# Kernel optimization log

Hardware: AMD Instinct MI355X
Metric: run time of the kernel (lower is better)

The kernel has to match this reference:

```python
import jax, jax.numpy as jnp
import numpy as np

N = 30000   # nodes
E = 300000  # edges
B = 64      # graphs
H = 4       # heads
C = 64      # channels per head
HC = H * C  # 256


def setup_inputs() -> dict:
    key = jax.random.key(0)
    ks = jax.random.split(key, 32)

    def rn(k, shape):
        scale = 1.0 / np.sqrt(shape[0])
        return (jax.random.normal(k, shape) * scale).astype(jnp.float32)

    inp = {}
    inp["x"] = jax.random.normal(ks[0], (N, 13), dtype=jnp.float32)
    inp["edge_index"] = jax.random.randint(ks[1], (2, E), 0, N, dtype=jnp.int64)
    inp["edge_attr"] = jax.random.normal(ks[2], (E, 51), dtype=jnp.float32)
    inp["batch"] = jnp.sort(jax.random.randint(ks[3], (N,), 0, B, dtype=jnp.int64))
    # init node MLP: Linear(13 -> 128) (plain_last => no act/norm)
    inp["W0"] = rn(ks[4], (13, 128)); inp["b0"] = jnp.zeros((128,), jnp.float32)
    # GATv2 layer 1: in 128 -> H=4, C=64
    inp["Wl1"] = rn(ks[5], (128, HC)); inp["bl1"] = jnp.zeros((HC,), jnp.float32)
    inp["Wr1"] = rn(ks[6], (128, HC)); inp["br1"] = jnp.zeros((HC,), jnp.float32)
    inp["We1"] = rn(ks[7], (51, HC))
    inp["att1"] = rn(ks[8], (H, C))
    inp["bias1"] = jnp.zeros((HC,), jnp.float32)
    # GATv2 layer 2: in 256 -> H=4, C=64
    inp["Wl2"] = rn(ks[9], (HC, HC)); inp["bl2"] = jnp.zeros((HC,), jnp.float32)
    inp["Wr2"] = rn(ks[10], (HC, HC)); inp["br2"] = jnp.zeros((HC,), jnp.float32)
    inp["We2"] = rn(ks[11], (51, HC))
    inp["att2"] = rn(ks[12], (H, C))
    inp["bias2"] = jnp.zeros((HC,), jnp.float32)
    # attention pooling MLP: Linear(256 -> 256) (plain_last)
    inp["Wp"] = rn(ks[13], (HC, HC)); inp["bp"] = jnp.zeros((HC,), jnp.float32)
    # out MLP: Linear(256->256)+BN+ReLU, Linear(256->2001)
    inp["Wo1"] = rn(ks[14], (HC, 256)); inp["bo1"] = jnp.zeros((256,), jnp.float32)
    inp["gamma"] = jnp.ones((256,), jnp.float32); inp["beta"] = jnp.zeros((256,), jnp.float32)
    inp["Wo2"] = rn(ks[15], (256, 2001)); inp["bo2"] = jnp.zeros((2001,), jnp.float32)
    return inp


def _gatv2(x, src, dst, ea, Wl, bl, Wr, br, We, att, bias):
    n = x.shape[0]
    xl = (x @ Wl + bl).reshape(n, H, C)   # source transform (also message content)
    xr = (x @ Wr + br).reshape(n, H, C)   # target transform
    ee = (ea @ We).reshape(-1, H, C)      # edge embedding, no bias
    z = jax.nn.leaky_relu(xl[src] + xr[dst] + ee, negative_slope=0.2)  # [E,H,C]
    logit = jnp.einsum('ehc,hc->eh', z, att)                           # [E,H]
    m = jax.ops.segment_max(logit, dst, num_segments=n)                # [N,H]
    w = jnp.exp(logit - m[dst])
    den = jax.ops.segment_sum(w, dst, num_segments=n)
    alpha = w / (den[dst] + 1e-16)                                     # segment softmax
    out = jax.ops.segment_sum(xl[src] * alpha[:, :, None], dst, num_segments=n)
    return out.reshape(n, HC) + bias


def _forward(x, edge_index, edge_attr, batch, W0, b0, Wl1, bl1, Wr1, br1, We1, att1, bias1,
             Wl2, bl2, Wr2, br2, We2, att2, bias2, Wp, bp, Wo1, bo1, gamma, beta, Wo2, bo2):
    src, dst = edge_index[0], edge_index[1]
    h = x @ W0 + b0
    h = _gatv2(h, src, dst, edge_attr, Wl1, bl1, Wr1, br1, We1, att1, bias1)
    h = _gatv2(h, src, dst, edge_attr, Wl2, bl2, Wr2, br2, We2, att2, bias2)
    # softmax attention pooling over nodes of each graph (per feature column)
    a = h @ Wp + bp                                       # [N,HC]
    am = jax.ops.segment_max(a, batch, num_segments=B)
    aw = jnp.exp(a - am[batch])
    ad = jax.ops.segment_sum(aw, batch, num_segments=B)
    attw = aw / (ad[batch] + 1e-16)
    g = jax.ops.segment_sum(h * attw, batch, num_segments=B)  # [B,HC]
    # out MLP: Linear + BatchNorm(train stats) + ReLU + Linear, then leaky_relu
    y = g @ Wo1 + bo1
    mu = jnp.mean(y, axis=0)
    var = jnp.var(y, axis=0)
    y = (y - mu) / jnp.sqrt(var + 1e-5) * gamma + beta
    y = jax.nn.relu(y)
    y = y @ Wo2 + bo2
    return jax.nn.leaky_relu(y, negative_slope=0.01)


def reference(x, edge_index, edge_attr, batch, W0, b0, Wl1, bl1, Wr1, br1, We1, att1, bias1,
              Wl2, bl2, Wr2, br2, We2, att2, bias2, Wp, bp, Wo1, bo1, gamma, beta, Wo2, bo2):
    return _forward(x, edge_index, edge_attr, batch, W0, b0, Wl1, bl1, Wr1, br1, We1, att1, bias1,
                    Wl2, bl2, Wr2, br2, We2, att2, bias2, Wp, bp, Wo1, bo1, gamma, beta, Wo2, bo2)
```

## Files before the change

### kernel.cpp

```cpp
#include <hip/hip_runtime.h>
#include <hip/hip_bf16.h>

#define NN 30000
#define EE 300000
#define BB 64
#define HH 4
#define CC 64
#define HC 256

typedef __attribute__((ext_vector_type(8))) short short8;
typedef __attribute__((ext_vector_type(4))) float floatx4;

__device__ __forceinline__ float b2f(short x) {
    return __uint_as_float(((unsigned)(unsigned short)x) << 16);
}
__device__ __forceinline__ unsigned short f2b(float f) {
    __hip_bfloat16 h = __float2bfloat16(f);
    return *(unsigned short*)&h;
}

#define GLD16(gp, lp) __builtin_amdgcn_global_load_lds( \
    (const __attribute__((address_space(1))) void*)(gp), \
    (__attribute__((address_space(3))) void*)(lp), 16, 0, 0)

#define ROT2(x) ((((x) << 2) | ((x) >> 3)) & 31)
#define EESWZ(chunk, row) (ROT2(chunk) ^ (((row) >> 2) & 3) ^ (((row) & 1) << 2))

template<int CT>
__global__ __launch_bounds__(256) void mfma_gemm(
    const ushort* __restrict__ A, const ushort* __restrict__ Bt,
    const float* __restrict__ bias, float* __restrict__ outF,
    __hip_bfloat16* __restrict__ outB, int M, int Nc, int K) {
    constexpr int SMEM_USHORTS =
        ((64 * 32 + CT * 64 * 32) > (64 * CT * 64)) ? (64 * 32 + CT * 64 * 32)
                                                    : (64 * CT * 64);
    __shared__ __align__(16) ushort smem[SMEM_USHORTS];
    ushort* lA = smem;
    ushort* lB = smem + 64 * 32;
    const int tid = threadIdx.x, lane = tid & 63, wv = tid >> 6;
    const int row0 = blockIdx.x * 64, col0 = blockIdx.y * (CT * 64);

    floatx4 acc[4][CT];
#pragma unroll
    for (int r = 0; r < 4; r++)
#pragma unroll
        for (int c = 0; c < CT; c++) acc[r][c] = (floatx4){0.f, 0.f, 0.f, 0.f};

    const int arow = tid >> 2;
    const int sl   = (tid & 3) ^ ((tid >> 3) & 3);
    const ushort* ga = A + (size_t)(row0 + arow) * K + sl * 8;
    const int m16 = lane & 15, q = lane >> 4;

    for (int k0 = 0; k0 < K; k0 += 32) {
        __syncthreads();
        GLD16(ga + k0, &lA[tid * 8]);
#pragma unroll
        for (int j = 0; j < CT; j++) {
            const ushort* gb = Bt + (size_t)(col0 + j * 64 + arow) * K + k0 + sl * 8;
            GLD16(gb, &lB[j * 2048 + tid * 8]);
        }
        __syncthreads();
        short8 aF[4], bF[CT];
#pragma unroll
        for (int r = 0; r < 4; r++) {
            int rr = r * 16 + m16;
            aF[r] = *(const short8*)&lA[rr * 32 + ((q ^ ((rr >> 1) & 3)) << 3)];
        }
#pragma unroll
        for (int c = 0; c < CT; c++) {
            int nr = (wv * CT + c) * 16 + m16;
            bF[c] = *(const short8*)&lB[nr * 32 + ((q ^ ((nr >> 1) & 3)) << 3)];
        }
#pragma unroll
        for (int r = 0; r < 4; r++)
#pragma unroll
            for (int c = 0; c < CT; c++)
                acc[r][c] = __builtin_amdgcn_mfma_f32_16x16x32_bf16(aF[r], bF[c], acc[r][c], 0, 0, 0);
    }

    if (outB != nullptr) {
        __syncthreads();
#pragma unroll
        for (int c = 0; c < CT; c++) {
            int lcol = (wv * CT + c) * 16 + m16;
            float bv = bias ? bias[col0 + lcol] : 0.f;
            int ch = lcol >> 3, c7 = lcol & 7;
#pragma unroll
            for (int r = 0; r < 4; r++)
#pragma unroll
                for (int j = 0; j < 4; j++) {
                    int row = r * 16 + q * 4 + j;
                    smem[row * (CT * 64) + ((ch ^ (row & 7)) << 3) + c7] =
                        f2b(acc[r][c][j] + bv);
                }
        }
        __syncthreads();
        constexpr int SH = (CT == 4) ? 5 : 4;
#pragma unroll
        for (int s = 0; s < CT * 2; s++) {
            int g = tid + 256 * s;
            int row = g >> SH, ch = g & (CT * 8 - 1);
            int grow = row0 + row;
            if (grow < M) {
                short8 v = *(const short8*)&smem[row * (CT * 64) + ((ch ^ (row & 7)) << 3)];
                *(short8*)((ushort*)outB + (size_t)grow * Nc + col0 + ch * 8) = v;
            }
        }
    } else {
#pragma unroll
        for (int c = 0; c < CT; c++) {
            int col = col0 + (wv * CT + c) * 16 + m16;
            float bv = bias ? bias[col] : 0.f;
#pragma unroll
            for (int r = 0; r < 4; r++)
#pragma unroll
                for (int j = 0; j < 4; j++) {
                    int row = row0 + r * 16 + q * 4 + j;
                    if (row < M) outF[(size_t)row * Nc + col] = acc[r][c][j] + bv;
                }
        }
    }
}

__global__ void permute_ea_frag(const float* __restrict__ ea,
                                const int* __restrict__ eidx,
                                ushort* __restrict__ ea_frag) {
    const int t = threadIdx.x, tile = blockIdx.x;
    const int r  = t >> 6;
    const int ch = (t >> 3) & 7;
    if (ch == 7) return;
    const int m0 = (t * 2) & 15;
    ushort* outp = ea_frag + (size_t)tile * 4096 + t * 16;
#pragma unroll
    for (int half = 0; half < 2; half++) {
        int row = r * 16 + m0 + half;
        int gi = tile * 64 + row;
        int e = (gi < EE) ? eidx[gi] : -1;
        short8 v8;
#pragma unroll
        for (int j = 0; j < 8; j++) {
            int k = ch * 8 + j;
            float v = (e >= 0 && k < 51) ? ea[(size_t)e * 51 + k] : 0.f;
            v8[j] = (short)f2b(v);
        }
        *(short8*)(outp + half * 8) = v8;
    }
}

__global__ void pack_we_frag(const float* __restrict__ WeA,
                             const float* __restrict__ WeB,
                             ushort* __restrict__ WfA, ushort* __restrict__ WfB) {
    const float* We = blockIdx.y ? WeB : WeA;
    ushort* Wf = blockIdx.y ? WfB : WfA;
    int o = blockIdx.x * 256 + threadIdx.x;
    int j = o & 7, m16 = (o >> 3) & 15, ch = (o >> 7) & 7, nt = o >> 10;
    int n = nt * 16 + m16, k = ch * 8 + j;
    float v = (k < 51) ? We[k * 256 + n] : 0.f;
    Wf[o] = f2b(v);
}

__global__ __launch_bounds__(256, 4) void edge_fused(
    const ushort* __restrict__ ea_frag, const ushort* __restrict__ Wfrag,
    const float* __restrict__ att,
    const int* __restrict__ src_csr, const int* __restrict__ dst_csr,
    const ushort* __restrict__ xlr, float* __restrict__ logitp) {
    __shared__ __align__(16) ushort eeS[64 * 256];
    __shared__ float satt[256];
    const int tid = threadIdx.x, lane = tid & 63, wv = tid >> 6;
    const int tile = ((int)blockIdx.x & 7) * 586 + ((int)blockIdx.x >> 3);
    const int i0 = tile * 64;
    satt[tid] = att[tid];
    const int m16 = lane & 15, q = lane >> 4;

    floatx4 acc[4][4];
#pragma unroll
    for (int r = 0; r < 4; r++)
#pragma unroll
        for (int c = 0; c < 4; c++) acc[r][c] = (floatx4){0.f, 0.f, 0.f, 0.f};

    short8 zz;
#pragma unroll
    for (int z = 0; z < 8; z++) zz[z] = 0;

    const ushort* af = ea_frag + (size_t)tile * 4096;
#pragma unroll
    for (int k0 = 0; k0 < 2; k0++) {
        short8 aF[4], bF[4];
        const bool live = !(k0 == 1 && q == 3);
        if (live) {
#pragma unroll
            for (int r = 0; r < 4; r++)
                aF[r] = *(const short8*)&af[((r * 8 + k0 * 4 + q) * 16 + m16) * 8];
#pragma unroll
            for (int c = 0; c < 4; c++)
                bF[c] = *(const short8*)&Wfrag[(((wv * 4 + c) * 8 + k0 * 4 + q) * 16 + m16) * 8];
        } else {
#pragma unroll
            for (int r = 0; r < 4; r++) aF[r] = zz;
#pragma unroll
            for (int c = 0; c < 4; c++) bF[c] = zz;
        }
#pragma unroll
        for (int r = 0; r < 4; r++)
#pragma unroll
            for (int c = 0; c < 4; c++)
                acc[r][c] = __builtin_amdgcn_mfma_f32_16x16x32_bf16(aF[r], bF[c], acc[r][c], 0, 0, 0);
    }

#pragma unroll
    for (int r = 0; r < 4; r++)
#pragma unroll
        for (int cc = 0; cc < 4; cc++)
#pragma unroll
            for (int j = 0; j < 4; j++) {
                int row = r * 16 + q * 4 + j;
                int col = (wv * 4 + cc) * 16 + m16;
                int chunk = col >> 3;
                int P = EESWZ(chunk, row);
                eeS[row * 256 + (P << 3) + (col & 7)] = f2b(acc[r][cc][j]);
            }
    __syncthreads();

    const int el = tid >> 2, h = tid & 3;
    const int i = i0 + el;
    if (i < EE) {
        int src = src_csr[i], dstn = dst_csr[i];
        const ushort* xlp = xlr + (size_t)src * 512 + h * 64;
        const ushort* xrp = xlr + (size_t)dstn * 512 + 256 + h * 64;
        float s = 0.f;
#pragma unroll
        for (int c = 0; c < 8; c++) {
            short8 xlv = *(const short8*)(xlp + c * 8);
            short8 xrv = *(const short8*)(xrp + c * 8);
            int chunk = h * 8 + c;
            int P = EESWZ(chunk, el);
            short8 eev = *(const short8*)&eeS[el * 256 + (P << 3)];
#pragma unroll
            for (int j = 0; j < 8; j++) {
                float v = b2f(xlv[j]) + b2f(xrv[j]) + b2f(eev[j]);
                v = v > 0.f ? v : 0.2f * v;
                s += v * satt[h * 64 + c * 8 + j];
            }
        }
        logitp[(size_t)i * 4 + h] = s;
    }
}

__global__ void pack_x(const float* __restrict__ x, __hip_bfloat16* __restrict__ d,
                       int* __restrict__ deg) {
    int i = blockIdx.x * 256 + threadIdx.x;
    if (i < NN) deg[i] = 0;
    if (i >= NN * 32) return;
    int n = i >> 5, k = i & 31;
    d[i] = __float2bfloat16(k < 13 ? x[n * 13 + k] : 0.f);
}
struct PackJob { const float* W; __hip_bfloat16* dst; int K, Nc, Kpad, rowoff; };
struct PackJobs { PackJob j[6]; };
__global__ void pack_all(PackJobs jobs) {
    PackJob jb = jobs.j[blockIdx.y];
    int tot = jb.Nc * jb.Kpad;
    for (int i = blockIdx.x * 256 + threadIdx.x; i < tot; i += gridDim.x * 256) {
        int n = i / jb.Kpad, k = i - n * jb.Kpad;
        float v = (k < jb.K) ? jb.W[k * jb.Nc + n] : 0.f;
        jb.dst[(size_t)(jb.rowoff + n) * jb.Kpad + k] = __float2bfloat16(v);
    }
}
__global__ void cat2(const float* __restrict__ a, const float* __restrict__ b,
                     float* __restrict__ o) {
    int i = blockIdx.x * 256 + threadIdx.x;
    if (i < 512) o[i] = i < 256 ? a[i] : b[i - 256];
}

__global__ void hist_deg(const int* __restrict__ ei, int* __restrict__ deg) {
    int e = blockIdx.x * 256 + threadIdx.x;
    if (e < EE) atomicAdd(&deg[ei[EE + e]], 1);
}
__global__ void scan1(const int* __restrict__ deg, int* __restrict__ partial,
                      int* __restrict__ bsum) {
    __shared__ int sh[256];
    int t = threadIdx.x, i = blockIdx.x * 256 + t;
    int v = (i < NN) ? deg[i] : 0;
    sh[t] = v; __syncthreads();
    for (int off = 1; off < 256; off <<= 1) {
        int x = (t >= off) ? sh[t - off] : 0;
        __syncthreads();
        sh[t] += x;
        __syncthreads();
    }
    if (i < NN) partial[i] = sh[t] - v;
    if (t == 255) bsum[blockIdx.x] = sh[255];
}
__global__ void scan2(int* __restrict__ bsum, int nb) {
    __shared__ int sh[256];
    int t = threadIdx.x;
    int v = (t < nb) ? bsum[t] : 0;
    sh[t] = v; __syncthreads();
    for (int off = 1; off < 256; off <<= 1) {
        int x = (t >= off) ? sh[t - off] : 0;
        __syncthreads();
        sh[t] += x;
        __syncthreads();
    }
    if (t < nb) bsum[t] = sh[t] - v;
}
__global__ void scan3(const int* __restrict__ partial, const int* __restrict__ bsum,
                      int* __restrict__ start, int* __restrict__ cursor) {
    int i = blockIdx.x * 256 + threadIdx.x;
    if (i < NN) { start[i] = partial[i] + bsum[i >> 8]; cursor[i] = 0; }
    else if (i == NN) start[NN] = EE;
}
__global__ void scatter_e(const int* __restrict__ ei, int* __restrict__ cursor,
                          const int* __restrict__ start, int* __restrict__ eidx,
                          int* __restrict__ src_csr, int* __restrict__ dst_csr) {
    int e = blockIdx.x * 256 + threadIdx.x;
    if (e >= EE) return;
    int s = ei[e];
    int d = ei[EE + e];
    int p = atomicAdd(&cursor[d], 1);
    int pos = start[d] + p;
    eidx[pos] = e;
    src_csr[pos] = s;
    dst_csr[pos] = d;
}

__global__ __launch_bounds__(256) void aggregate_csr(
    const ushort* __restrict__ xlr, const float* __restrict__ logitp,
    const int* __restrict__ src_csr, const int* __restrict__ start,
    const float* __restrict__ bias, ushort* __restrict__ outb) {
    const int lane = threadIdx.x & 63, wv = threadIdx.x >> 6;
    const int dst = blockIdx.x * 4 + wv;
    if (dst >= NN) return;
    const int s0 = start[dst];
    const int deg = start[dst + 1] - s0;
    const int h = lane >> 4;

    float m[4] = {-3.4e38f, -3.4e38f, -3.4e38f, -3.4e38f};
    float lg[4] = {0.f, 0.f, 0.f, 0.f};
    int mysrc = 0;
    if (lane < deg) {
        mysrc = src_csr[s0 + lane];
        float4 l4 = ((const float4*)logitp)[s0 + lane];
        lg[0] = l4.x; lg[1] = l4.y; lg[2] = l4.z; lg[3] = l4.w;
        m[0] = l4.x; m[1] = l4.y; m[2] = l4.z; m[3] = l4.w;
    }
    for (int i = 64 + lane; i < deg; i += 64) {
        float4 l4 = ((const float4*)logitp)[s0 + i];
        m[0] = fmaxf(m[0], l4.x); m[1] = fmaxf(m[1], l4.y);
        m[2] = fmaxf(m[2], l4.z); m[3] = fmaxf(m[3], l4.w);
    }
#pragma unroll
    for (int off = 32; off; off >>= 1)
#pragma unroll
        for (int k = 0; k < 4; k++) m[k] = fmaxf(m[k], __shfl_xor(m[k], off));

    float w[4], d[4];
#pragma unroll
    for (int k = 0; k < 4; k++) {
        w[k] = (lane < deg) ? __expf(lg[k] - m[k]) : 0.f;
        d[k] = w[k];
    }
    for (int i = 64 + lane; i < deg; i += 64) {
        float4 l4 = ((const float4*)logitp)[s0 + i];
        d[0] += __expf(l4.x - m[0]); d[1] += __expf(l4.y - m[1]);
        d[2] += __expf(l4.z - m[2]); d[3] += __expf(l4.w - m[3]);
    }
#pragma unroll
    for (int off = 32; off; off >>= 1)
#pragma unroll
        for (int k = 0; k < 4; k++) d[k] += __shfl_xor(d[k], off);
    const float dh = 1.f / (((h == 0) ? d[0] : (h == 1) ? d[1] : (h == 2) ? d[2] : d[3]) + 1e-16f);
    const float mh = (h == 0) ? m[0] : (h == 1) ? m[1] : (h == 2) ? m[2] : m[3];

    float4 b4 = ((const float4*)bias)[lane];
    float a0 = b4.x, a1 = b4.y, a2 = b4.z, a3 = b4.w;

    const int dcap = deg < 64 ? deg : 64;
    const ushort* xbase = xlr + (size_t)lane * 4;
    int i = 0;
    for (; i + 4 <= dcap; i += 4) {
        int sv[4]; float aw[4];
#pragma unroll
        for (int u = 0; u < 4; u++) {
            sv[u] = __shfl(mysrc, i + u);
            float s0v = __shfl(w[0], i + u), s1v = __shfl(w[1], i + u);
            float s2v = __shfl(w[2], i + u), s3v = __shfl(w[3], i + u);
            aw[u] = ((h == 0) ? s0v : (h == 1) ? s1v : (h == 2) ? s2v : s3v) * dh;
        }
        ushort4 xv[4];
#pragma unroll
        for (int u = 0; u < 4; u++)
            xv[u] = *(const ushort4*)(xbase + (size_t)sv[u] * 512);
#pragma unroll
        for (int u = 0; u < 4; u++) {
            a0 += b2f(xv[u].x) * aw[u]; a1 += b2f(xv[u].y) * aw[u];
            a2 += b2f(xv[u].z) * aw[u]; a3 += b2f(xv[u].w) * aw[u];
        }
    }
    for (; i < dcap; i++) {
        int srcv = __shfl(mysrc, i);
        float s0v = __shfl(w[0], i), s1v = __shfl(w[1], i);
        float s2v = __shfl(w[2], i), s3v = __shfl(w[3], i);
        float aw = ((h == 0) ? s0v : (h == 1) ? s1v : (h == 2) ? s2v : s3v) * dh;
        ushort4 xv = *(const ushort4*)(xbase + (size_t)srcv * 512);
        a0 += b2f(xv.x) * aw; a1 += b2f(xv.y) * aw;
        a2 += b2f(xv.z) * aw; a3 += b2f(xv.w) * aw;
    }
    for (int ii = 64; ii < deg; ii++) {
        int srcv = src_csr[s0 + ii];
        float4 l4 = ((const float4*)logitp)[s0 + ii];
        float lh = (h == 0) ? l4.x : (h == 1) ? l4.y : (h == 2) ? l4.z : l4.w;
        float aw = __expf(lh - mh) * dh;
        ushort4 xv = *(const ushort4*)(xbase + (size_t)srcv * 512);
        a0 += b2f(xv.x) * aw; a1 += b2f(xv.y) * aw;
        a2 += b2f(xv.z) * aw; a3 += b2f(xv.w) * aw;
    }
    ushort4 ov;
    ov.x = f2b(a0); ov.y = f2b(a1); ov.z = f2b(a2); ov.w = f2b(a3);
    *(ushort4*)(outb + (size_t)dst * 256 + lane * 4) = ov;
}

__device__ __forceinline__ unsigned fmap(float f) {
    unsigned u = __float_as_uint(f);
    return (u & 0x80000000u) ? ~u : (u | 0x80000000u);
}
__device__ __forceinline__ float funmap(unsigned u) {
    return (u & 0x80000000u) ? __uint_as_float(u & 0x7FFFFFFFu)
                             : __uint_as_float(~u);
}

__global__ void pool_max(const float* __restrict__ a, const int* __restrict__ batch,
                         unsigned* __restrict__ am, float* __restrict__ den,
                         float* __restrict__ num) {
    const int c = threadIdx.x;
    if (blockIdx.x < BB) {
        den[blockIdx.x * HC + c] = 0.f;
        num[blockIdx.x * HC + c] = 0.f;
    }
    const int n0 = blockIdx.x * 64;
    int curb = batch[n0];
    float m = -3.4e38f;
    const int nend = min(n0 + 64, NN);
    for (int n = n0; n < nend; n++) {
        int b = batch[n];
        float v = a[(size_t)n * HC + c];
        if (b != curb) { atomicMax(&am[curb * HC + c], fmap(m)); curb = b; m = v; }
        else           { m = fmaxf(m, v); }
    }
    atomicMax(&am[curb * HC + c], fmap(m));
}
__global__ void pool_sums(const float* __restrict__ a, const __hip_bfloat16* __restrict__ h2,
                          const int* __restrict__ batch, const unsigned* __restrict__ am,
                          float* __restrict__ den, float* __restrict__ num) {
    const int c = threadIdx.x;
    const int n0 = blockIdx.x * 64;
    int curb = batch[n0];
    float sd = 0.f, sn = 0.f;
    float mcur = funmap(am[curb * HC + c]);
    const int nend = min(n0 + 64, NN);
    for (int n = n0; n < nend; n++) {
        int b = batch[n];
        if (b != curb) {
            atomicAdd(&den[curb * HC + c], sd);
            atomicAdd(&num[curb * HC + c], sn);
            curb = b; sd = 0.f; sn = 0.f; mcur = funmap(am[b * HC + c]);
        }
        float w = __expf(a[(size_t)n * HC + c] - mcur);
        sd += w;
        sn += __bfloat162float(h2[(size_t)n * HC + c]) * w;
    }
    atomicAdd(&den[curb * HC + c], sd);
    atomicAdd(&num[curb * HC + c], sn);
}

__global__ void mlp_lin1(const float* __restrict__ num, const float* __restrict__ den,
                         const float* __restrict__ Wo1, const float* __restrict__ bo1,
                         float* __restrict__ y) {
    __shared__ float gsh[HC];
    const int c = threadIdx.x;
    const int r = blockIdx.x;
    gsh[c] = num[r * HC + c] / (den[r * HC + c] + 1e-16f);
    __syncthreads();
    float acc = bo1[c];
#pragma unroll 4
    for (int k = 0; k < HC; k++) acc = fmaf(gsh[k], Wo1[k * HC + c], acc);
    y[r * HC + c] = acc;
}
__global__ void bn_relu(float* __restrict__ y, const float* __restrict__ gamma,
                        const float* __restrict__ beta) {
    const int c = threadIdx.x;
    float s = 0.f, sq = 0.f;
    for (int r = 0; r < BB; r++) { float v = y[r * HC + c]; s += v; sq += v * v; }
    float mu  = s * (1.f / BB);
    float var = sq * (1.f / BB) - mu * mu;
    float inv = rsqrtf(var + 1e-5f) * gamma[c];
    float bt  = beta[c];
    for (int r = 0; r < BB; r++) {
        float v = (y[r * HC + c] - mu) * inv + bt;
        y[r * HC + c] = v > 0.f ? v : 0.f;
    }
}
__global__ void mlp_lin2(const float* __restrict__ y, const float* __restrict__ Wo2,
                         const float* __restrict__ bo2, float* __restrict__ out) {
    const int j = blockIdx.x * 256 + threadIdx.x;
    const int r = blockIdx.y;
    if (j >= 2001) return;
    float acc = bo2[j];
#pragma unroll 4
    for (int k = 0; k < HC; k++) acc = fmaf(y[r * HC + k], Wo2[k * 2001 + j], acc);
    out[r * 2001 + j] = acc > 0.f ? acc : 0.01f * acc;
}

extern "C" void kernel_launch(void* const* d_in, const int* in_sizes, int n_in,
                              void* d_out, int out_size, void* d_ws, size_t ws_size,
                              hipStream_t stream) {
    const float* x     = (const float*)d_in[0];
    const int*   ei    = (const int*)d_in[1];
    const float* ea    = (const float*)d_in[2];
    const int*   batch = (const int*)d_in[3];
    const float* W0 = (const float*)d_in[4];  const float* b0 = (const float*)d_in[5];
    const float* Wl1 = (const float*)d_in[6]; const float* bl1 = (const float*)d_in[7];
    const float* Wr1 = (const float*)d_in[8]; const float* br1 = (const float*)d_in[9];
    const float* We1 = (const float*)d_in[10]; const float* att1 = (const float*)d_in[11];
    const float* bias1 = (const float*)d_in[12];
    const float* Wl2 = (const float*)d_in[13]; const float* bl2 = (const float*)d_in[14];
    const float* Wr2 = (const float*)d_in[15]; const float* br2 = (const float*)d_in[16];
    const float* We2 = (const float*)d_in[17]; const float* att2 = (const float*)d_in[18];
    const float* bias2 = (const float*)d_in[19];
    const float* Wp = (const float*)d_in[20]; const float* bp = (const float*)d_in[21];
    const float* Wo1 = (const float*)d_in[22]; const float* bo1 = (const float*)d_in[23];
    const float* gamma = (const float*)d_in[24]; const float* beta = (const float*)d_in[25];
    const float* Wo2 = (const float*)d_in[26]; const float* bo2 = (const float*)d_in[27];
    float* out = (float*)d_out;

    char* p = (char*)d_ws;
    auto alloc = [&](size_t bytes) { char* r = p; p += (bytes + 255) & ~(size_t)255; return r; };
    const int MP = 30016;
    const int ET = 4688;
    __hip_bfloat16* xpad  = (__hip_bfloat16*)alloc((size_t)MP * 32 * 2);
    __hip_bfloat16* W0t   = (__hip_bfloat16*)alloc(128 * 32 * 2);
    __hip_bfloat16* W1t   = (__hip_bfloat16*)alloc(512 * 128 * 2);
    __hip_bfloat16* W2t   = (__hip_bfloat16*)alloc(512 * 256 * 2);
    __hip_bfloat16* Wpt   = (__hip_bfloat16*)alloc(256 * 256 * 2);
    ushort* Wef1 = (ushort*)alloc(256 * 64 * 2);
    ushort* Wef2 = (ushort*)alloc(256 * 64 * 2);
    float* bcat1 = (float*)alloc(512 * 4);
    float* bcat2 = (float*)alloc(512 * 4);
    __hip_bfloat16* h0b  = (__hip_bfloat16*)alloc((size_t)MP * 128 * 2);
    __hip_bfloat16* xlrb = (__hip_bfloat16*)alloc((size_t)MP * 512 * 2);
    __hip_bfloat16* h1b  = (__hip_bfloat16*)alloc((size_t)MP * 256 * 2);
    __hip_bfloat16* h2b  = (__hip_bfloat16*)alloc((size_t)MP * 256 * 2);
    ushort* ea_frag = (ushort*)alloc((size_t)ET * 4096 * 2);
    float* abuf = (float*)alloc((size_t)MP * 256 * 4);
    float* logit = (float*)alloc((size_t)EE * 4 * 4);
    int* deg    = (int*)alloc(NN * 4);
    int* cursor = (int*)alloc(NN * 4);
    int* partial= (int*)alloc(NN * 4);
    int* bsum   = (int*)alloc(256 * 4);
    int* start  = (int*)alloc((NN + 4) * 4);
    int* eidx   = (int*)alloc((size_t)EE * 4);
    int* src_csr= (int*)alloc((size_t)EE * 4);
    int* dst_csr= (int*)alloc((size_t)EE * 4);
    unsigned* am = (unsigned*)alloc(BB * HC * 4);
    float* den  = (float*)alloc(BB * HC * 4);
    float* num  = (float*)alloc(BB * HC * 4);
    float* ybuf = (float*)alloc(BB * HC * 4);

    const int NB = (NN + 255) / 256;

    pack_x<<<(NN * 32 + 255) / 256, 256, 0, stream>>>(x, xpad, deg);
    PackJobs pj;
    pj.j[0] = {W0,  W0t, 13, 128, 32, 0};
    pj.j[1] = {Wl1, W1t, 128, 256, 128, 0};
    pj.j[2] = {Wr1, W1t, 128, 256, 128, 256};
    pj.j[3] = {Wl2, W2t, 256, 256, 256, 0};
    pj.j[4] = {Wr2, W2t, 256, 256, 256, 256};
    pj.j[5] = {Wp,  Wpt, 256, 256, 256, 0};
    pack_all<<<dim3(64, 6), 256, 0, stream>>>(pj);
    pack_we_frag<<<dim3(64, 2), 256, 0, stream>>>(We1, We2, Wef1, Wef2);
    cat2<<<2, 256, 0, stream>>>(bl1, br1, bcat1);
    cat2<<<2, 256, 0, stream>>>(bl2, br2, bcat2);

    hist_deg<<<(EE + 255) / 256, 256, 0, stream>>>(ei, deg);
    scan1<<<NB, 256, 0, stream>>>(deg, partial, bsum);
    scan2<<<1, 256, 0, stream>>>(bsum, NB);
    scan3<<<NB + 1, 256, 0, stream>>>(partial, bsum, start, cursor);
    scatter_e<<<(EE + 255) / 256, 256, 0, stream>>>(ei, cursor, start, eidx, src_csr, dst_csr);
    permute_ea_frag<<<ET, 256, 0, stream>>>(ea, eidx, ea_frag);

    mfma_gemm<2><<<dim3(469, 1), 256, 0, stream>>>(
        (const ushort*)xpad, (const ushort*)W0t, b0, nullptr, h0b, NN, 128, 32);

    mfma_gemm<4><<<dim3(469, 2), 256, 0, stream>>>(
        (const ushort*)h0b, (const ushort*)W1t, bcat1, nullptr, xlrb, NN, 512, 128);
    edge_fused<<<ET, 256, 0, stream>>>(ea_frag, Wef1, att1, src_csr, dst_csr,
                                       (const ushort*)xlrb, logit);
    aggregate_csr<<<(NN + 3) / 4, 256, 0, stream>>>(
        (const ushort*)xlrb, logit, src_csr, start, bias1, (ushort*)h1b);

    mfma_gemm<4><<<dim3(469, 2), 256, 0, stream>>>(
        (const ushort*)h1b, (const ushort*)W2t, bcat2, nullptr, xlrb, NN, 512, 256);
    edge_fused<<<ET, 256, 0, stream>>>(ea_frag, Wef2, att2, src_csr, dst_csr,
                                       (const ushort*)xlrb, logit);
    aggregate_csr<<<(NN + 3) / 4, 256, 0, stream>>>(
        (const ushort*)xlrb, logit, src_csr, start, bias2, (ushort*)h2b);

    mfma_gemm<4><<<dim3(469, 1), 256, 0, stream>>>(
        (const ushort*)h2b, (const ushort*)Wpt, bp, abuf, nullptr, NN, 256, 256);
    hipMemsetAsync(am, 0, BB * HC * 4, stream);
    const int poolGrid = (NN + 63) / 64;
    pool_max<<<poolGrid, HC, 0, stream>>>(abuf, batch, am, den, num);
    pool_sums<<<poolGrid, HC, 0, stream>>>(abuf, h2b, batch, am, den, num);

    mlp_lin1<<<BB, HC, 0, stream>>>(num, den, Wo1, bo1, ybuf);
    bn_relu<<<1, HC, 0, stream>>>(ybuf, gamma, beta);
    mlp_lin2<<<dim3(8, BB), 256, 0, stream>>>(ybuf, Wo2, bo2, out);
}
```

Baseline: 598.4 us.

## Prefetch source features before edge MFMA, store pool logits in bf16, merge launches

The edge kernel now issues the gather of source-node features before the edge-embedding MFMA stage, so that global-memory latency overlaps with the matrix work. This costs extra registers, so the launch bounds drop from 4 to 3 waves per SIMD. The pooling GEMM writes its output in bf16 instead of fp32, halving the traffic read by the two pooling kernels at some precision cost. The am zeroing is folded into hist_deg, replacing a memset, and the two cat2 launches are merged into one to cut launch overhead.

```diff
diff --git a/kernel.cpp b/kernel.cpp
--- a/kernel.cpp
+++ b/kernel.cpp
@@ -159,7 +159,7 @@
     Wf[o] = f2b(v);
 }
 
-__global__ __launch_bounds__(256, 4) void edge_fused(
+__global__ __launch_bounds__(256, 3) void edge_fused(
     const ushort* __restrict__ ea_frag, const ushort* __restrict__ Wfrag,
     const float* __restrict__ att,
     const int* __restrict__ src_csr, const int* __restrict__ dst_csr,
@@ -172,6 +172,16 @@
     satt[tid] = att[tid];
     const int m16 = lane & 15, q = lane >> 4;
 
+    const int el = tid >> 2, h = tid & 3;
+    const int i = i0 + el;
+    const bool live_e = (i < EE);
+    const int ic = live_e ? i : (EE - 1);
+    const int src = src_csr[ic], dstn = dst_csr[ic];
+    const ushort* xlp = xlr + (size_t)src * 512 + h * 64;
+    short8 xlv[8];
+#pragma unroll
+    for (int c = 0; c < 8; c++) xlv[c] = *(const short8*)(xlp + c * 8);
+
     floatx4 acc[4][4];
 #pragma unroll
     for (int r = 0; r < 4; r++)
@@ -221,23 +231,18 @@
             }
     __syncthreads();
 
-    const int el = tid >> 2, h = tid & 3;
-    const int i = i0 + el;
-    if (i < EE) {
-        int src = src_csr[i], dstn = dst_csr[i];
-        const ushort* xlp = xlr + (size_t)src * 512 + h * 64;
+    if (live_e) {
         const ushort* xrp = xlr + (size_t)dstn * 512 + 256 + h * 64;
         float s = 0.f;
 #pragma unroll
         for (int c = 0; c < 8; c++) {
-            short8 xlv = *(const short8*)(xlp + c * 8);
             short8 xrv = *(const short8*)(xrp + c * 8);
             int chunk = h * 8 + c;
             int P = EESWZ(chunk, el);
             short8 eev = *(const short8*)&eeS[el * 256 + (P << 3)];
 #pragma unroll
             for (int j = 0; j < 8; j++) {
-                float v = b2f(xlv[j]) + b2f(xrv[j]) + b2f(eev[j]);
+                float v = b2f(xlv[c][j]) + b2f(xrv[j]) + b2f(eev[j]);
                 v = v > 0.f ? v : 0.2f * v;
                 s += v * satt[h * 64 + c * 8 + j];
             }
@@ -265,14 +270,20 @@
         jb.dst[(size_t)(jb.rowoff + n) * jb.Kpad + k] = __float2bfloat16(v);
     }
 }
-__global__ void cat2(const float* __restrict__ a, const float* __restrict__ b,
-                     float* __restrict__ o) {
+__global__ void cat2(const float* __restrict__ a1, const float* __restrict__ b1,
+                     float* __restrict__ o1, const float* __restrict__ a2,
+                     const float* __restrict__ b2, float* __restrict__ o2) {
     int i = blockIdx.x * 256 + threadIdx.x;
+    const float* a = blockIdx.y ? a2 : a1;
+    const float* b = blockIdx.y ? b2 : b1;
+    float* o = blockIdx.y ? o2 : o1;
     if (i < 512) o[i] = i < 256 ? a[i] : b[i - 256];
 }
 
-__global__ void hist_deg(const int* __restrict__ ei, int* __restrict__ deg) {
+__global__ void hist_deg(const int* __restrict__ ei, int* __restrict__ deg,
+                         unsigned* __restrict__ am) {
     int e = blockIdx.x * 256 + threadIdx.x;
+    if (e < BB * HC) am[e] = 0u;
     if (e < EE) atomicAdd(&deg[ei[EE + e]], 1);
 }
 __global__ void scan1(const int* __restrict__ deg, int* __restrict__ partial,
@@ -428,7 +439,7 @@
                              : __uint_as_float(~u);
 }
 
-__global__ void pool_max(const float* __restrict__ a, const int* __restrict__ batch,
+__global__ void pool_max(const __hip_bfloat16* __restrict__ a, const int* __restrict__ batch,
                          unsigned* __restrict__ am, float* __restrict__ den,
                          float* __restrict__ num) {
     const int c = threadIdx.x;
@@ -442,13 +453,14 @@
     const int nend = min(n0 + 64, NN);
     for (int n = n0; n < nend; n++) {
         int b = batch[n];
-        float v = a[(size_t)n * HC + c];
+        float v = __bfloat162float(a[(size_t)n * HC + c]);
         if (b != curb) { atomicMax(&am[curb * HC + c], fmap(m)); curb = b; m = v; }
         else           { m = fmaxf(m, v); }
     }
     atomicMax(&am[curb * HC + c], fmap(m));
 }
-__global__ void pool_sums(const float* __restrict__ a, const __hip_bfloat16* __restrict__ h2,
+__global__ void pool_sums(const __hip_bfloat16* __restrict__ a,
+                          const __hip_bfloat16* __restrict__ h2,
                           const int* __restrict__ batch, const unsigned* __restrict__ am,
                           float* __restrict__ den, float* __restrict__ num) {
     const int c = threadIdx.x;
@@ -464,7 +476,7 @@
             atomicAdd(&num[curb * HC + c], sn);
             curb = b; sd = 0.f; sn = 0.f; mcur = funmap(am[b * HC + c]);
         }
-        float w = __expf(a[(size_t)n * HC + c] - mcur);
+        float w = __expf(__bfloat162float(a[(size_t)n * HC + c]) - mcur);
         sd += w;
         sn += __bfloat162float(h2[(size_t)n * HC + c]) * w;
     }
@@ -550,7 +562,7 @@
     __hip_bfloat16* h1b  = (__hip_bfloat16*)alloc((size_t)MP * 256 * 2);
     __hip_bfloat16* h2b  = (__hip_bfloat16*)alloc((size_t)MP * 256 * 2);
     ushort* ea_frag = (ushort*)alloc((size_t)ET * 4096 * 2);
-    float* abuf = (float*)alloc((size_t)MP * 256 * 4);
+    __hip_bfloat16* abuf = (__hip_bfloat16*)alloc((size_t)MP * 256 * 2);
     float* logit = (float*)alloc((size_t)EE * 4 * 4);
     int* deg    = (int*)alloc(NN * 4);
     int* cursor = (int*)alloc(NN * 4);
@@ -577,10 +589,9 @@
     pj.j[5] = {Wp,  Wpt, 256, 256, 256, 0};
     pack_all<<<dim3(64, 6), 256, 0, stream>>>(pj);
     pack_we_frag<<<dim3(64, 2), 256, 0, stream>>>(We1, We2, Wef1, Wef2);
-    cat2<<<2, 256, 0, stream>>>(bl1, br1, bcat1);
-    cat2<<<2, 256, 0, stream>>>(bl2, br2, bcat2);
-
-    hist_deg<<<(EE + 255) / 256, 256, 0, stream>>>(ei, deg);
+    cat2<<<dim3(2, 2), 256, 0, stream>>>(bl1, br1, bcat1, bl2, br2, bcat2);
+
+    hist_deg<<<(EE + 255) / 256, 256, 0, stream>>>(ei, deg, am);
     scan1<<<NB, 256, 0, stream>>>(deg, partial, bsum);
     scan2<<<1, 256, 0, stream>>>(bsum, NB);
     scan3<<<NB + 1, 256, 0, stream>>>(partial, bsum, start, cursor);
@@ -605,8 +616,7 @@
         (const ushort*)xlrb, logit, src_csr, start, bias2, (ushort*)h2b);
 
     mfma_gemm<4><<<dim3(469, 1), 256, 0, stream>>>(
-        (const ushort*)h2b, (const ushort*)Wpt, bp, abuf, nullptr, NN, 256, 256);
-    hipMemsetAsync(am, 0, BB * HC * 4, stream);
+        (const ushort*)h2b, (const ushort*)Wpt, bp, nullptr, abuf, NN, 256, 256);
     const int poolGrid = (NN + 63) / 64;
     pool_max<<<poolGrid, HC, 0, stream>>>(abuf, batch, am, den, num);
     pool_sums<<<poolGrid, HC, 0, stream>>>(abuf, h2b, batch, am, den, num);
```

Result: faster. 581.0 us (-2.9%).
